# Kernel tuning notes

Hardware: AMD Instinct MI355X
Metric: run time of the kernel (lower is better)

The kernel has to match this reference:

```python
import jax, jax.numpy as jnp
import numpy as np

B, S, HID = 2, 2048, 2048
H, KVH, D = 16, 4, 128
GROUPS = H // KVH  # 4


def apply_rotary(x, cos, sin):
    # x: [B, h, S, D]; cos/sin: [S, D//2]
    xr = x[..., 0::2]
    xi = x[..., 1::2]
    c = cos[None, None, :, :]
    s = sin[None, None, :, :]
    orr = xr * c - xi * s
    oi = xr * s + xi * c
    return jnp.stack([orr, oi], axis=-1).reshape(x.shape)


def setup_inputs() -> dict:
    key = jax.random.key(0)
    k0, k1, k2, k3, k4 = jax.random.split(key, 5)
    x = jax.random.normal(k0, (B, S, HID), dtype=jnp.float32)
    # real RoPE frequencies (llama-style), stored as [S, D//2, 2] = (cos, sin)
    inv_freq = 1.0 / (10000.0 ** (np.arange(0, D, 2, dtype=np.float32) / D))
    t = np.arange(S, dtype=np.float32)
    ang = np.outer(t, inv_freq)  # [S, D//2]
    freqs_cis = jnp.asarray(np.stack([np.cos(ang), np.sin(ang)], axis=-1), dtype=jnp.float32)
    sc = 0.02
    wq = jax.random.normal(k1, (HID, H * D), dtype=jnp.float32) * sc
    wk = jax.random.normal(k2, (HID, KVH * D), dtype=jnp.float32) * sc
    wv = jax.random.normal(k3, (HID, KVH * D), dtype=jnp.float32) * sc
    wo = jax.random.normal(k4, (H * D, HID), dtype=jnp.float32) * sc
    return {"x": x, "freqs_cis": freqs_cis, "wq": wq, "wk": wk, "wv": wv, "wo": wo}


def reference(x, freqs_cis, wq, wk, wv, wo):
    b, s, _ = x.shape
    cos, sin = freqs_cis[..., 0], freqs_cis[..., 1]
    q = (x @ wq).reshape(b, s, H, D).transpose(0, 2, 1, 3)    # [B,H,S,D]
    k = (x @ wk).reshape(b, s, KVH, D).transpose(0, 2, 1, 3)  # [B,KVH,S,D]
    v = (x @ wv).reshape(b, s, KVH, D).transpose(0, 2, 1, 3)
    q = apply_rotary(q, cos, sin)
    k = apply_rotary(k, cos, sin)
    # GQA expand: repeat kv heads into query-head groups
    k = jnp.repeat(k, GROUPS, axis=1)  # [B,H,S,D]
    v = jnp.repeat(v, GROUPS, axis=1)
    scale = 1.0 / jnp.sqrt(jnp.asarray(D, dtype=x.dtype))
    scores = jnp.einsum("bhqd,bhkd->bhqk", q, k) * scale
    causal = jnp.tril(jnp.ones((s, s), dtype=bool))
    scores = jnp.where(causal[None, None], scores, jnp.asarray(-jnp.inf, dtype=scores.dtype))
    attn = jax.nn.softmax(scores, axis=-1)
    out = jnp.einsum("bhqk,bhkd->bhqd", attn, v)
    out = out.transpose(0, 2, 1, 3).reshape(b, s, H * D)
    return out @ wo
```

## Files before the change

### kernel.cpp

```cpp
#include <hip/hip_runtime.h>
#include <hip/hip_bf16.h>

#define B_   2
#define S_   2048
#define HID_ 2048
#define H_   16
#define KVH_ 4
#define D_   128
#define M_   4096
#define NQKV 3072

typedef __attribute__((ext_vector_type(8))) short bf16x8;
typedef __attribute__((ext_vector_type(4))) float f32x4;
typedef const __attribute__((address_space(1))) unsigned int* gas_p;
typedef __attribute__((address_space(3))) unsigned int* las_p;

__device__ __forceinline__ unsigned short f2b(float f) {
    __hip_bfloat16 h = __float2bfloat16(f);
    return *reinterpret_cast<unsigned short*>(&h);
}
__device__ __forceinline__ float b2f(unsigned short u) {
    __hip_bfloat16 h;
    *reinterpret_cast<unsigned short*>(&h) = u;
    return __bfloat162float(h);
}

__global__ __launch_bounds__(256)
void convert_all(const float* __restrict__ x,
                 const float* __restrict__ wq, const float* __restrict__ wk,
                 const float* __restrict__ wv, const float* __restrict__ wo,
                 unsigned short* __restrict__ xb,
                 unsigned short* __restrict__ wqkvT,
                 unsigned short* __restrict__ woT) {
    int z = blockIdx.z;
    if (z >= 4) {
        int lin = ((z - 4) * 64 + blockIdx.y) * 64 + blockIdx.x;
        int i = (lin * 256 + threadIdx.x) * 4;
        float4 v = *(const float4*)(x + i);
        ushort4 o;
        o.x = f2b(v.x); o.y = f2b(v.y); o.z = f2b(v.z); o.w = f2b(v.w);
        *(ushort4*)(xb + i) = o;
        return;
    }
    __shared__ float tile[32][33];
    const float* w; int N, nbase; unsigned short* dst;
    if (z == 0)      { w = wq; N = 2048; nbase = 0;    dst = wqkvT; }
    else if (z == 1) { w = wk; N = 512;  nbase = 2048; dst = wqkvT; }
    else if (z == 2) { w = wv; N = 512;  nbase = 2560; dst = wqkvT; }
    else             { w = wo; N = 2048; nbase = 0;    dst = woT; }
    int n0 = blockIdx.x * 32, k0 = blockIdx.y * 32;
    if (n0 >= N) return;
    int tx = threadIdx.x & 31, ty = threadIdx.x >> 5;
    #pragma unroll
    for (int j = 0; j < 4; j++)
        tile[ty + j*8][tx] = w[(size_t)(k0 + ty + j*8) * N + n0 + tx];
    __syncthreads();
    #pragma unroll
    for (int j = 0; j < 4; j++)
        dst[(size_t)(nbase + n0 + ty + j*8) * 2048 + k0 + tx] = f2b(tile[tx][ty + j*8]);
}

#define BAR    asm volatile("s_barrier" ::: "memory")
#define LG0    do { asm volatile("s_waitcnt lgkmcnt(0)" ::: "memory"); \
                    __builtin_amdgcn_sched_barrier(0); } while (0)
#define GATE0  asm volatile("s_waitcnt vmcnt(0)" ::: "memory")
#define GATE6  asm volatile("s_waitcnt vmcnt(6)" ::: "memory")
#define GATE7  asm volatile("s_waitcnt vmcnt(7)" ::: "memory")
#define PHI    __builtin_amdgcn_s_setprio(1)
#define PLO    __builtin_amdgcn_s_setprio(0)

#define STG(srcrow, ldsbase, half, tile) do {                                   \
    _Pragma("unroll")                                                           \
    for (int it_ = 0; it_ < 2; ++it_) {                                         \
      int p_ = w * 128 + it_ * 64 + lane;                                       \
      int r_ = (half) * 128 + (p_ >> 3);                                        \
      int q8_ = ((p_ & 7) ^ ((p_ >> 3) & 7)) * 8;                               \
      __builtin_amdgcn_global_load_lds(                                         \
          (gas_p)((srcrow) + (size_t)r_ * 2048 + (tile) * 64 + q8_),            \
          (las_p)((char*)(ldsbase) + ((half) * 1024 + w * 128 + it_ * 64) * 16),\
          16, 0, 0);                                                            \
    } } while (0)

#define STGB(srcrow, ldsbase, unit, tile) do {                                  \
      int p_ = w * 64 + lane;                                                   \
      int r_ = (unit) * 64 + (p_ >> 3);                                         \
      int q8_ = ((p_ & 7) ^ ((p_ >> 3) & 7)) * 8;                               \
      __builtin_amdgcn_global_load_lds(                                         \
          (gas_p)((srcrow) + (size_t)r_ * 2048 + (tile) * 64 + q8_),            \
          (las_p)((char*)(ldsbase) + ((unit) * 512 + p_) * 16),                 \
          16, 0, 0);                                                            \
    } while (0)

#define RDAq(dst, bufi) do {                                                    \
    const unsigned short* Ab_ = &As[bufi][0] + wr*4096 + l15*64;                \
    _Pragma("unroll")                                                           \
    for (int f_ = 0; f_ < 4; ++f_) {                                            \
      dst[f_][0] = *(const bf16x8*)(Ab_ + f_*1024 + slot0);                     \
      dst[f_][1] = *(const bf16x8*)(Ab_ + f_*1024 + slot1);                     \
    } } while (0)

#define RDBq(dst, bufi, nh) do {                                                \
    const unsigned short* Bb_ = &Bs[bufi][0] + wc*6144 + (nh)*3072 + l15*64;    \
    _Pragma("unroll")                                                           \
    for (int g_ = 0; g_ < 3; ++g_) {                                            \
      dst[g_][0] = *(const bf16x8*)(Bb_ + g_*1024 + slot0);                     \
      dst[g_][1] = *(const bf16x8*)(Bb_ + g_*1024 + slot1);                     \
    } } while (0)

#define MMq(mh, rb, nh) do {                                                    \
    _Pragma("unroll")                                                           \
    for (int f_ = 2*(mh); f_ < 2*(mh)+2; ++f_)                                  \
      _Pragma("unroll")                                                         \
      for (int g_ = 0; g_ < 3; ++g_) {                                          \
        acc[f_][(nh)*3+g_] = __builtin_amdgcn_mfma_f32_16x16x32_bf16(           \
            ra[f_][0], rb[g_][0], acc[f_][(nh)*3+g_], 0, 0, 0);                 \
        acc[f_][(nh)*3+g_] = __builtin_amdgcn_mfma_f32_16x16x32_bf16(           \
            ra[f_][1], rb[g_][1], acc[f_][(nh)*3+g_], 0, 0, 0);                 \
      } } while (0)

__global__ __launch_bounds__(512)
void gemm8(const unsigned short* __restrict__ A,
           const unsigned short* __restrict__ BT,
           unsigned short* __restrict__ qkvb,
           unsigned short* __restrict__ vTb,
           const float* __restrict__ freqs) {
    __shared__ unsigned short As[2][16384];
    __shared__ unsigned short Bs[2][12288];

    int tid  = threadIdx.x;
    int lane = tid & 63, w = tid >> 6;
    int l15  = lane & 15, quad = lane >> 4;
    int wr = w >> 1, wc = w & 1;
    int bid = blockIdx.y * 16 + blockIdx.x;
    int s_  = (bid & 7) * 32 + (bid >> 3);
    int by  = s_ >> 4, bx = s_ & 15;
    int row0 = by * 256, col0 = bx * 192;
    int slot0 = (quad ^ (lane & 7)) * 8;
    int slot1 = slot0 ^ 32;

    const unsigned short* Arow = A  + (size_t)row0 * 2048;
    const unsigned short* Brow = BT + (size_t)col0 * 2048;

    f32x4 acc[4][6];
    #pragma unroll
    for (int i = 0; i < 4; ++i)
        #pragma unroll
        for (int j = 0; j < 6; ++j) acc[i][j] = f32x4{0.f, 0.f, 0.f, 0.f};

    bf16x8 ra[4][2];
    bf16x8 rbl[3][2];
    bf16x8 rbh[3][2];

    STG (Arow, &As[0][0], 0, 0);
    STG (Arow, &As[0][0], 1, 0);
    STGB(Brow, &Bs[0][0], 0, 0);
    STGB(Brow, &Bs[0][0], 1, 0);
    STGB(Brow, &Bs[0][0], 2, 0);
    STG (Arow, &As[1][0], 0, 1);
    STG (Arow, &As[1][0], 1, 1);
    STGB(Brow, &Bs[1][0], 0, 1);
    STGB(Brow, &Bs[1][0], 1, 1);
    STGB(Brow, &Bs[1][0], 2, 1);
    GATE7;
    BAR;

    #pragma unroll 1
    for (int i = 0; i < 15; ++i) {
        int t = 2 * i;
        RDAq(ra, 0); RDBq(rbl, 0, 0);
        BAR; LG0; PHI; MMq(0, rbl, 0); PLO; BAR;
        RDBq(rbh, 0, 1); STG(Arow, &As[0][0], 0, t + 2);
        BAR; LG0; PHI; MMq(0, rbh, 1); PLO; BAR;
        STG(Arow, &As[0][0], 1, t + 2);
        BAR; LG0; PHI; MMq(1, rbl, 0); PLO; BAR;
        STGB(Brow, &Bs[0][0], 0, t + 2);
        STGB(Brow, &Bs[0][0], 1, t + 2);
        STGB(Brow, &Bs[0][0], 2, t + 2);
        BAR; LG0; PHI; MMq(1, rbh, 1); PLO; GATE7; BAR;
        RDAq(ra, 1); RDBq(rbl, 1, 0);
        BAR; LG0; PHI; MMq(0, rbl, 0); PLO; BAR;
        RDBq(rbh, 1, 1); STG(Arow, &As[1][0], 0, t + 3);
        BAR; LG0; PHI; MMq(0, rbh, 1); PLO; BAR;
        STG(Arow, &As[1][0], 1, t + 3);
        BAR; LG0; PHI; MMq(1, rbl, 0); PLO; BAR;
        STGB(Brow, &Bs[1][0], 0, t + 3);
        STGB(Brow, &Bs[1][0], 1, t + 3);
        STGB(Brow, &Bs[1][0], 2, t + 3);
        BAR; LG0; PHI; MMq(1, rbh, 1); PLO; GATE7; BAR;
    }
    RDAq(ra, 0); RDBq(rbl, 0, 0);
    BAR; LG0; PHI; MMq(0, rbl, 0); PLO; BAR;
    RDBq(rbh, 0, 1);
    BAR; LG0; PHI; MMq(0, rbh, 1); PLO; BAR;
    BAR; LG0; PHI; MMq(1, rbl, 0); PLO; BAR;
    BAR; LG0; PHI; MMq(1, rbh, 1); PLO; GATE0; BAR;
    RDAq(ra, 1); RDBq(rbl, 1, 0);
    BAR; LG0; PHI; MMq(0, rbl, 0); PLO; BAR;
    RDBq(rbh, 1, 1);
    BAR; LG0; PHI; MMq(0, rbh, 1); PLO; BAR;
    BAR; LG0; PHI; MMq(1, rbl, 0); PLO; BAR;
    LG0; PHI; MMq(1, rbh, 1); PLO;

    int q4 = quad * 4;
    const float qscale = 0.08838834764831845f;
    #pragma unroll
    for (int f = 0; f < 4; ++f) {
        int mb = row0 + wr*64 + f*16 + q4;
        #pragma unroll
        for (int g = 0; g < 6; ++g) {
            int colbase = col0 + wc*96 + g*16;
            int colb = colbase + l15;
            if (colbase < 2560) {
                int dd = (colb & 127) & ~1;
                bool odd = colb & 1;
                float sc = (colbase < 2048) ? qscale : 1.f;
                #pragma unroll
                for (int rr = 0; rr < 4; ++rr) {
                    int m = mb + rr;
                    int s = m & 2047;
                    float v  = acc[f][g][rr];
                    float pv = __shfl_xor(v, 1);
                    float cs = freqs[s*128 + dd];
                    float sn = freqs[s*128 + dd + 1];
                    float o  = odd ? (pv*sn + v*cs) : (v*cs - pv*sn);
                    qkvb[(size_t)m * NQKV + colb] = f2b(o * sc);
                }
            } else {
                int vrow = (row0 >> 11) * 512 + (colb - 2560);
                int s0 = mb & 2047;
                ushort4 ov;
                ov.x = f2b(acc[f][g][0]);
                ov.y = f2b(acc[f][g][1]);
                ov.z = f2b(acc[f][g][2]);
                ov.w = f2b(acc[f][g][3]);
                *(ushort4*)(vTb + (size_t)vrow * 2048 + s0) = ov;
            }
        }
    }
}

#define RDAo(bufi) do {                                                         \
    const unsigned short* Ab_ = &As[bufi][0] + wr * 4096 + l15 * 64;            \
    _Pragma("unroll")                                                           \
    for (int f_ = 0; f_ < 4; ++f_) {                                            \
      af[f_][0] = *(const bf16x8*)(Ab_ + f_ * 1024 + slot0);                    \
      af[f_][1] = *(const bf16x8*)(Ab_ + f_ * 1024 + slot1);                    \
    } } while (0)

#define RDBo(bufi, g) do {                                                      \
    const unsigned short* Bb_ = &Bs[bufi][0] + wc * 4096 + l15 * 64;            \
    bfr[g][0] = *(const bf16x8*)(Bb_ + (g) * 1024 + slot0);                     \
    bfr[g][1] = *(const bf16x8*)(Bb_ + (g) * 1024 + slot1);                     \
    } while (0)

#define MM8o(mi, ni) do {                                                       \
    _Pragma("unroll")                                                           \
    for (int f_ = 2*(mi); f_ < 2*(mi)+2; ++f_)                                  \
      _Pragma("unroll")                                                         \
      for (int g_ = 2*(ni); g_ < 2*(ni)+2; ++g_) {                              \
        acc[f_][g_] = __builtin_amdgcn_mfma_f32_16x16x32_bf16(                  \
            af[f_][0], bfr[g_][0], acc[f_][g_], 0, 0, 0);                       \
        acc[f_][g_] = __builtin_amdgcn_mfma_f32_16x16x32_bf16(                  \
            af[f_][1], bfr[g_][1], acc[f_][g_], 0, 0, 0);                       \
      } } while (0)

__global__ __launch_bounds__(512)
void gemm8o(const unsigned short* __restrict__ A,
            const unsigned short* __restrict__ BT,
            float* __restrict__ Cf) {
    __shared__ unsigned short As[2][16384];
    __shared__ unsigned short Bs[2][8192];

    int tid  = threadIdx.x;
    int lane = tid & 63, w = tid >> 6;
    int l15  = lane & 15, quad = lane >> 4;
    int wr = w >> 1, wc = w & 1;
    int bid = blockIdx.y * 16 + blockIdx.x;
    int s_  = (bid & 7) * 32 + (bid >> 3);
    int by  = s_ >> 4, bx = s_ & 15;
    int row0 = by * 256, col0 = bx * 128;
    int slot0 = (quad ^ (lane & 7)) * 8;
    int slot1 = slot0 ^ 32;

    const unsigned short* Arow = A  + (size_t)row0 * 2048;
    const unsigned short* Brow = BT + (size_t)col0 * 2048;

    f32x4 acc[4][4];
    #pragma unroll
    for (int i = 0; i < 4; ++i)
        #pragma unroll
        for (int j = 0; j < 4; ++j) acc[i][j] = f32x4{0.f, 0.f, 0.f, 0.f};

    bf16x8 af[4][2];
    bf16x8 bfr[4][2];

    STG(Arow, &As[0][0], 0, 0);
    STG(Arow, &As[0][0], 1, 0);
    STG(Brow, &Bs[0][0], 0, 0);
    STG(Arow, &As[1][0], 0, 1);
    STG(Arow, &As[1][0], 1, 1);
    STG(Brow, &Bs[1][0], 0, 1);
    GATE6;
    BAR;

    #pragma unroll 1
    for (int i = 0; i < 15; ++i) {
        int t = 2 * i;
        RDAo(0); RDBo(0, 0); RDBo(0, 1);
        BAR; LG0; PHI; MM8o(0, 0); PLO; BAR;
        RDBo(0, 2); RDBo(0, 3); STG(Arow, &As[0][0], 0, t + 2);
        BAR; LG0; PHI; MM8o(0, 1); PLO; BAR;
        STG(Arow, &As[0][0], 1, t + 2);
        BAR; LG0; PHI; MM8o(1, 0); PLO; BAR;
        STG(Brow, &Bs[0][0], 0, t + 2);
        BAR; LG0; PHI; MM8o(1, 1); PLO; GATE6; BAR;
        RDAo(1); RDBo(1, 0); RDBo(1, 1);
        BAR; LG0; PHI; MM8o(0, 0); PLO; BAR;
        RDBo(1, 2); RDBo(1, 3); STG(Arow, &As[1][0], 0, t + 3);
        BAR; LG0; PHI; MM8o(0, 1); PLO; BAR;
        STG(Arow, &As[1][0], 1, t + 3);
        BAR; LG0; PHI; MM8o(1, 0); PLO; BAR;
        STG(Brow, &Bs[1][0], 0, t + 3);
        BAR; LG0; PHI; MM8o(1, 1); PLO; GATE6; BAR;
    }
    RDAo(0); RDBo(0, 0); RDBo(0, 1);
    BAR; LG0; PHI; MM8o(0, 0); PLO; BAR;
    RDBo(0, 2); RDBo(0, 3);
    BAR; LG0; PHI; MM8o(0, 1); PLO; BAR;
    BAR; LG0; PHI; MM8o(1, 0); PLO; BAR;
    BAR; LG0; PHI; MM8o(1, 1); PLO; GATE0; BAR;
    RDAo(1); RDBo(1, 0); RDBo(1, 1);
    BAR; LG0; PHI; MM8o(0, 0); PLO; BAR;
    RDBo(1, 2); RDBo(1, 3);
    BAR; LG0; PHI; MM8o(0, 1); PLO; BAR;
    BAR; LG0; PHI; MM8o(1, 0); PLO; BAR;
    LG0; PHI; MM8o(1, 1); PLO;

    int q4 = quad * 4;
    #pragma unroll
    for (int f = 0; f < 4; ++f) {
        int mb = row0 + wr*64 + f*16 + q4;
        #pragma unroll
        for (int g = 0; g < 4; ++g) {
            int colb = col0 + wc*64 + g*16 + l15;
            #pragma unroll
            for (int rr = 0; rr < 4; ++rr)
                Cf[(size_t)(mb + rr) * 2048 + colb] = acc[f][g][rr];
        }
    }
}

__global__ __launch_bounds__(512)
void attn_mfma(const unsigned short* __restrict__ qkv,
               const unsigned short* __restrict__ vT,
               unsigned short* __restrict__ ao,
               unsigned short* __restrict__ wsP,
               float2* __restrict__ wsML) {
    __shared__ unsigned short Ks[64 * 128];
    __shared__ unsigned short Vt[128 * 64];

    int tid  = threadIdx.x;
    int lane = tid & 63, w = tid >> 6;
    int quad = lane >> 4, l15 = lane & 15;
    int hw = w >> 1, qhalf = w & 1;
    int bx = blockIdx.x, hk = blockIdx.y, b = blockIdx.z;
    int h = hk * 4 + hw;

    int qt, c;
    if (bx < 12)      { qt = 31 - bx / 3;        c = bx % 3; }
    else if (bx < 40) { qt = 27 - (bx - 12) / 2; c = (bx - 12) & 1; }
    else              { qt = 53 - bx;            c = 0; }
    int nt = qt + 1;
    int nch = (qt >= 28) ? 3 : (qt >= 14 ? 2 : 1);
    int kt_begin = c * 14;
    int kt_end = (nt < (c + 1) * 14) ? nt : (c + 1) * 14;
    bool lastc = (c == nch - 1);
    int q0 = qt * 64;

    bf16x8 aq[2][4];
    #pragma unroll
    for (int qf = 0; qf < 2; qf++) {
        const unsigned short* qrow =
            qkv + (size_t)(b*2048 + q0 + qhalf*32 + qf*16 + l15) * NQKV + h*128;
        #pragma unroll
        for (int k4 = 0; k4 < 4; k4++)
            aq[qf][k4] = *(const bf16x8*)(qrow + k4*32 + quad*8);
    }

    int koff[4][4];
    #pragma unroll
    for (int j = 0; j < 4; j++) {
        int row = ((j >> 1) * 32) + ((l15 >> 2) * 8) + ((j & 1) * 4) + (l15 & 3);
        #pragma unroll
        for (int k4 = 0; k4 < 4; k4++) {
            int slot = (k4 * 4 + quad) ^ (row & 15);
            koff[j][k4] = (row * 16 + slot) * 8;
        }
    }
    int vbase0 = (l15 * 8 + (quad ^ (l15 & 7))) * 8;
    int vbase1 = (l15 * 8 + ((4 + quad) ^ (l15 & 7))) * 8;

    const unsigned short* kb0 = qkv + (size_t)(b*2048) * NQKV + 2048 + hk*128;
    const unsigned short* vb0 = vT + (size_t)(b*512 + hk*128) * 2048;

    auto stage_k = [&](int kt) {
        #pragma unroll
        for (int it = 0; it < 2; it++) {
            int s = w * 128 + it * 64 + lane;
            int r = s >> 4, qp = s & 15;
            int q = qp ^ (r & 15);
            __builtin_amdgcn_global_load_lds(
                (gas_p)(kb0 + (size_t)(kt*64 + r) * NQKV + q * 8),
                (las_p)((char*)&Ks[0] + (w * 128 + it * 64) * 16),
                16, 0, 0);
        }
    };
    auto stage_v = [&](int kt) {
        #pragma unroll
        for (int it = 0; it < 2; it++) {
            int s = w * 128 + it * 64 + lane;
            int r = s >> 3, qp = s & 7;
            int q = qp ^ (r & 7);
            __builtin_amdgcn_global_load_lds(
                (gas_p)(vb0 + (size_t)r * 2048 + kt*64 + q * 8),
                (las_p)((char*)&Vt[0] + (w * 128 + it * 64) * 16),
                16, 0, 0);
        }
    };

    f32x4 o_acc[2][8];
    const f32x4 zf = {0.f, 0.f, 0.f, 0.f};
    #pragma unroll
    for (int qf = 0; qf < 2; qf++)
        #pragma unroll
        for (int jn = 0; jn < 8; jn++) o_acc[qf][jn] = zf;
    float m_i[2] = {-1e30f, -1e30f}, l_i[2] = {0.f, 0.f};
    int qglob[2] = {q0 + qhalf*32 + l15, q0 + qhalf*32 + 16 + l15};

    stage_k(kt_begin);
    for (int kt = kt_begin; kt < kt_end; kt++) {
        __syncthreads();
        stage_v(kt);

        f32x4 s_acc[2][4];
        #pragma unroll
        for (int j = 0; j < 4; j++) {
            s_acc[0][j] = zf; s_acc[1][j] = zf;
            #pragma unroll
            for (int k4 = 0; k4 < 4; k4++) {
                bf16x8 ak = *(const bf16x8*)&Ks[koff[j][k4]];
                s_acc[0][j] = __builtin_amdgcn_mfma_f32_16x16x32_bf16(ak, aq[0][k4], s_acc[0][j], 0, 0, 0);
                s_acc[1][j] = __builtin_amdgcn_mfma_f32_16x16x32_bf16(ak, aq[1][k4], s_acc[1][j], 0, 0, 0);
            }
        }

        bf16x8 pp[2][2];
        #pragma unroll
        for (int qf = 0; qf < 2; qf++) {
            float sv[4][4];
            #pragma unroll
            for (int j = 0; j < 4; j++)
                #pragma unroll
                for (int r = 0; r < 4; r++)
                    sv[j][r] = s_acc[qf][j][r];
            if (kt == qt) {
                #pragma unroll
                for (int j = 0; j < 4; j++)
                    #pragma unroll
                    for (int r = 0; r < 4; r++) {
                        int sloc = ((j >> 1) * 32) + quad*8 + ((j & 1) * 4) + r;
                        if (kt*64 + sloc > qglob[qf]) sv[j][r] = -1e30f;
                    }
            }
            float mx = sv[0][0];
            #pragma unroll
            for (int j = 0; j < 4; j++)
                #pragma unroll
                for (int r = 0; r < 4; r++) mx = fmaxf(mx, sv[j][r]);
            mx = fmaxf(mx, __shfl_xor(mx, 16));
            mx = fmaxf(mx, __shfl_xor(mx, 32));
            int defer = __all(mx <= m_i[qf] + 8.f);
            float mnew = defer ? m_i[qf] : fmaxf(m_i[qf], mx);
            float rs = 0.f;
            float p[4][4];
            #pragma unroll
            for (int j = 0; j < 4; j++)
                #pragma unroll
                for (int r = 0; r < 4; r++) {
                    p[j][r] = __expf(sv[j][r] - mnew);
                    rs += p[j][r];
                }
            if (!defer) {
                float alpha = __expf(m_i[qf] - mnew);
                l_i[qf] *= alpha;
                #pragma unroll
                for (int jn = 0; jn < 8; jn++)
                    #pragma unroll
                    for (int r = 0; r < 4; r++) o_acc[qf][jn][r] *= alpha;
                m_i[qf] = mnew;
            }
            l_i[qf] += rs;
            #pragma unroll
            for (int r = 0; r < 4; r++) {
                pp[qf][0][r]     = (short)f2b(p[0][r]);
                pp[qf][0][r + 4] = (short)f2b(p[1][r]);
                pp[qf][1][r]     = (short)f2b(p[2][r]);
                pp[qf][1][r + 4] = (short)f2b(p[3][r]);
            }
        }

        __syncthreads();
        if (kt + 1 < kt_end) stage_k(kt + 1);

        #pragma unroll
        for (int jn = 0; jn < 8; jn++) {
            bf16x8 av0 = *(const bf16x8*)&Vt[jn*1024 + vbase0];
            bf16x8 av1 = *(const bf16x8*)&Vt[jn*1024 + vbase1];
            o_acc[0][jn] = __builtin_amdgcn_mfma_f32_16x16x32_bf16(av0, pp[0][0], o_acc[0][jn], 0, 0, 0);
            o_acc[0][jn] = __builtin_amdgcn_mfma_f32_16x16x32_bf16(av1, pp[0][1], o_acc[0][jn], 0, 0, 0);
            o_acc[1][jn] = __builtin_amdgcn_mfma_f32_16x16x32_bf16(av0, pp[1][0], o_acc[1][jn], 0, 0, 0);
            o_acc[1][jn] = __builtin_amdgcn_mfma_f32_16x16x32_bf16(av1, pp[1][1], o_acc[1][jn], 0, 0, 0);
        }
    }

    int pi = 0, mi = 0;
    if (qt >= 14) {
        if (qt < 28) { mi = (qt - 14) * 2 + c;       pi = qt - 14; }
        else         { mi = 28 + (qt - 28) * 3 + c;  pi = 14 + (qt - 28) * 2 + c; }
    }
    #pragma unroll
    for (int qf = 0; qf < 2; qf++) {
        float lt = l_i[qf];
        lt += __shfl_xor(lt, 16);
        lt += __shfl_xor(lt, 32);
        float inv = 1.f / lt;
        int q_local = qhalf * 32 + qf * 16 + l15;
        unsigned short* dst;
        if (lastc)
            dst = ao + (size_t)(b*2048 + q0 + q_local) * 2048 + h*128;
        else
            dst = wsP + (size_t)(((pi * 8 + hk * 2 + b) * 4 + hw) * 64 + q_local) * 128;
        #pragma unroll
        for (int jn = 0; jn < 8; jn++) {
            ushort4 ov;
            ov.x = f2b(o_acc[qf][jn][0] * inv);
            ov.y = f2b(o_acc[qf][jn][1] * inv);
            ov.z = f2b(o_acc[qf][jn][2] * inv);
            ov.w = f2b(o_acc[qf][jn][3] * inv);
            *(ushort4*)(dst + jn*16 + quad*4) = ov;
        }
        if (qt >= 14 && quad == 0)
            wsML[(mi * 8 + hk * 2 + b) * 256 + hw * 64 + q_local]
                = make_float2(m_i[qf], lt);
    }
}

__global__ __launch_bounds__(256)
void merge_kernel(unsigned short* __restrict__ ao,
                  const unsigned short* __restrict__ wsP,
                  const float2* __restrict__ wsML) {
    int t = blockIdx.x * 256 + threadIdx.x;
    int d = (t & 15) * 8;
    int h = (t >> 4) & 15;
    int rest = t >> 8;
    int q_off = rest % 1152;
    int b = rest / 1152;
    int q = 896 + q_off;
    int qt = q >> 6, q_local = q & 63;
    int hk = h >> 2, hw = h & 3;
    int nch = (qt >= 28) ? 3 : 2;

    float mv[3], lv[3];
    for (int cc = 0; cc < nch; cc++) {
        int mi = (qt < 28) ? (qt - 14) * 2 + cc : 28 + (qt - 28) * 3 + cc;
        float2 ml = wsML[(mi * 8 + hk * 2 + b) * 256 + hw * 64 + q_local];
        mv[cc] = ml.x; lv[cc] = ml.y;
    }
    float M = mv[0];
    for (int cc = 1; cc < nch; cc++) M = fmaxf(M, mv[cc]);
    float f[3], S = 0.f;
    for (int cc = 0; cc < nch; cc++) { f[cc] = __expf(mv[cc] - M) * lv[cc]; S += f[cc]; }
    float inv = 1.f / S;

    unsigned short* arow = ao + (size_t)(b*2048 + q) * 2048 + h*128 + d;
    float outv[8];
    {
        ushort4 a0 = *(ushort4*)arow, a1 = *(ushort4*)(arow + 4);
        float fl = f[nch-1];
        outv[0] = fl*b2f(a0.x); outv[1] = fl*b2f(a0.y);
        outv[2] = fl*b2f(a0.z); outv[3] = fl*b2f(a0.w);
        outv[4] = fl*b2f(a1.x); outv[5] = fl*b2f(a1.y);
        outv[6] = fl*b2f(a1.z); outv[7] = fl*b2f(a1.w);
    }
    for (int cc = 0; cc < nch - 1; cc++) {
        int pi = (qt < 28) ? (qt - 14) : 14 + (qt - 28) * 2 + cc;
        const unsigned short* prow =
            wsP + (size_t)(((pi * 8 + hk * 2 + b) * 4 + hw) * 64 + q_local) * 128 + d;
        ushort4 p0 = *(const ushort4*)prow, p1 = *(const ushort4*)(prow + 4);
        float fc = f[cc];
        outv[0] += fc*b2f(p0.x); outv[1] += fc*b2f(p0.y);
        outv[2] += fc*b2f(p0.z); outv[3] += fc*b2f(p0.w);
        outv[4] += fc*b2f(p1.x); outv[5] += fc*b2f(p1.y);
        outv[6] += fc*b2f(p1.z); outv[7] += fc*b2f(p1.w);
    }
    ushort4 o0, o1;
    o0.x = f2b(outv[0]*inv); o0.y = f2b(outv[1]*inv);
    o0.z = f2b(outv[2]*inv); o0.w = f2b(outv[3]*inv);
    o1.x = f2b(outv[4]*inv); o1.y = f2b(outv[5]*inv);
    o1.z = f2b(outv[6]*inv); o1.w = f2b(outv[7]*inv);
    *(ushort4*)arow = o0;
    *(ushort4*)(arow + 4) = o1;
}

extern "C" void kernel_launch(void* const* d_in, const int* in_sizes, int n_in,
                              void* d_out, int out_size, void* d_ws, size_t ws_size,
                              hipStream_t stream) {
    const float* x     = (const float*)d_in[0];
    const float* freqs = (const float*)d_in[1];
    const float* wq    = (const float*)d_in[2];
    const float* wk    = (const float*)d_in[3];
    const float* wv    = (const float*)d_in[4];
    const float* wo    = (const float*)d_in[5];
    float* out = (float*)d_out;

    char* ws = (char*)d_ws;
    unsigned short* xbf    = (unsigned short*)(ws);
    unsigned short* aobuf  = (unsigned short*)(ws);
    unsigned short* wqkvT  = (unsigned short*)(ws + (16u<<20));
    unsigned short* woT    = (unsigned short*)(ws + (28u<<20));
    unsigned short* qkvbuf = (unsigned short*)(ws + (36u<<20));
    unsigned short* vTbuf  = (unsigned short*)(ws + (60u<<20));
    unsigned short* wsP  = (unsigned short*)(ws + (16u<<20));
    float2*         wsML = (float2*)(ws + (16u<<20) + 176u*65536u);

    convert_all<<<dim3(64, 64, 6), dim3(256), 0, stream>>>(
        x, wq, wk, wv, wo, xbf, wqkvT, woT);
    gemm8<<<dim3(16, 16), dim3(512), 0, stream>>>(
        xbf, wqkvT, qkvbuf, vTbuf, freqs);
    attn_mfma<<<dim3(54, 4, 2), dim3(512), 0, stream>>>(qkvbuf, vTbuf, aobuf, wsP, wsML);
    merge_kernel<<<2304, dim3(256), 0, stream>>>(aobuf, wsP, wsML);
    gemm8o<<<dim3(2048/128, M_/256), dim3(512), 0, stream>>>(aobuf, woT, out);
}
```

Before: 293.4 us.

## Double-buffer K/V tiles in attention with two-ahead async prefetch

The attention kernel's shared K and V tiles become two-slot ping-pong buffers. Both tiles are prefetched two iterations ahead with async global-to-LDS loads, and a vmcnt(4) wait before the barrier guarantees only the next tile has landed. This replaces the old scheme, where V was loaded at the start of each iteration and K between the softmax and PV phases, each behind a __syncthreads. The aim is to hide global-load latency behind the MFMA work. The cost is double the LDS footprint, which may reduce occupancy, plus redundant clamped loads on the final iterations of each chunk.

```diff
diff --git a/kernel.cpp b/kernel.cpp
--- a/kernel.cpp
+++ b/kernel.cpp
@@ -64,6 +64,7 @@
 #define LG0    do { asm volatile("s_waitcnt lgkmcnt(0)" ::: "memory"); \
                     __builtin_amdgcn_sched_barrier(0); } while (0)
 #define GATE0  asm volatile("s_waitcnt vmcnt(0)" ::: "memory")
+#define GATE4  asm volatile("s_waitcnt vmcnt(4)" ::: "memory")
 #define GATE6  asm volatile("s_waitcnt vmcnt(6)" ::: "memory")
 #define GATE7  asm volatile("s_waitcnt vmcnt(7)" ::: "memory")
 #define PHI    __builtin_amdgcn_s_setprio(1)
@@ -356,8 +357,8 @@
                unsigned short* __restrict__ ao,
                unsigned short* __restrict__ wsP,
                float2* __restrict__ wsML) {
-    __shared__ unsigned short Ks[64 * 128];
-    __shared__ unsigned short Vt[128 * 64];
+    __shared__ unsigned short Ks[2][64 * 128];
+    __shared__ unsigned short Vt[2][128 * 64];
 
     int tid  = threadIdx.x;
     int lane = tid & 63, w = tid >> 6;
@@ -403,7 +404,7 @@
     const unsigned short* kb0 = qkv + (size_t)(b*2048) * NQKV + 2048 + hk*128;
     const unsigned short* vb0 = vT + (size_t)(b*512 + hk*128) * 2048;
 
-    auto stage_k = [&](int kt) {
+    auto stage_k = [&](int bf, int kt) {
         #pragma unroll
         for (int it = 0; it < 2; it++) {
             int s = w * 128 + it * 64 + lane;
@@ -411,11 +412,11 @@
             int q = qp ^ (r & 15);
             __builtin_amdgcn_global_load_lds(
                 (gas_p)(kb0 + (size_t)(kt*64 + r) * NQKV + q * 8),
-                (las_p)((char*)&Ks[0] + (w * 128 + it * 64) * 16),
+                (las_p)((char*)&Ks[bf][0] + (w * 128 + it * 64) * 16),
                 16, 0, 0);
         }
     };
-    auto stage_v = [&](int kt) {
+    auto stage_v = [&](int bf, int kt) {
         #pragma unroll
         for (int it = 0; it < 2; it++) {
             int s = w * 128 + it * 64 + lane;
@@ -423,7 +424,7 @@
             int q = qp ^ (r & 7);
             __builtin_amdgcn_global_load_lds(
                 (gas_p)(vb0 + (size_t)r * 2048 + kt*64 + q * 8),
-                (las_p)((char*)&Vt[0] + (w * 128 + it * 64) * 16),
+                (las_p)((char*)&Vt[bf][0] + (w * 128 + it * 64) * 16),
                 16, 0, 0);
         }
     };
@@ -437,18 +438,21 @@
     float m_i[2] = {-1e30f, -1e30f}, l_i[2] = {0.f, 0.f};
     int qglob[2] = {q0 + qhalf*32 + l15, q0 + qhalf*32 + 16 + l15};
 
-    stage_k(kt_begin);
+    int kt1 = (kt_begin + 1 < kt_end) ? kt_begin + 1 : kt_begin;
+    stage_k(0, kt_begin); stage_v(0, kt_begin);
+    stage_k(1, kt1);      stage_v(1, kt1);
+    GATE4;
+    BAR;
+
+    int p = 0;
     for (int kt = kt_begin; kt < kt_end; kt++) {
-        __syncthreads();
-        stage_v(kt);
-
         f32x4 s_acc[2][4];
         #pragma unroll
         for (int j = 0; j < 4; j++) {
             s_acc[0][j] = zf; s_acc[1][j] = zf;
             #pragma unroll
             for (int k4 = 0; k4 < 4; k4++) {
-                bf16x8 ak = *(const bf16x8*)&Ks[koff[j][k4]];
+                bf16x8 ak = *(const bf16x8*)&Ks[p][koff[j][k4]];
                 s_acc[0][j] = __builtin_amdgcn_mfma_f32_16x16x32_bf16(ak, aq[0][k4], s_acc[0][j], 0, 0, 0);
                 s_acc[1][j] = __builtin_amdgcn_mfma_f32_16x16x32_bf16(ak, aq[1][k4], s_acc[1][j], 0, 0, 0);
             }
@@ -482,13 +486,13 @@
             int defer = __all(mx <= m_i[qf] + 8.f);
             float mnew = defer ? m_i[qf] : fmaxf(m_i[qf], mx);
             float rs = 0.f;
-            float p[4][4];
+            float pexp[4][4];
             #pragma unroll
             for (int j = 0; j < 4; j++)
                 #pragma unroll
                 for (int r = 0; r < 4; r++) {
-                    p[j][r] = __expf(sv[j][r] - mnew);
-                    rs += p[j][r];
+                    pexp[j][r] = __expf(sv[j][r] - mnew);
+                    rs += pexp[j][r];
                 }
             if (!defer) {
                 float alpha = __expf(m_i[qf] - mnew);
@@ -502,25 +506,29 @@
             l_i[qf] += rs;
             #pragma unroll
             for (int r = 0; r < 4; r++) {
-                pp[qf][0][r]     = (short)f2b(p[0][r]);
-                pp[qf][0][r + 4] = (short)f2b(p[1][r]);
-                pp[qf][1][r]     = (short)f2b(p[2][r]);
-                pp[qf][1][r + 4] = (short)f2b(p[3][r]);
+                pp[qf][0][r]     = (short)f2b(pexp[0][r]);
+                pp[qf][0][r + 4] = (short)f2b(pexp[1][r]);
+                pp[qf][1][r]     = (short)f2b(pexp[2][r]);
+                pp[qf][1][r + 4] = (short)f2b(pexp[3][r]);
             }
         }
 
-        __syncthreads();
-        if (kt + 1 < kt_end) stage_k(kt + 1);
-
         #pragma unroll
         for (int jn = 0; jn < 8; jn++) {
-            bf16x8 av0 = *(const bf16x8*)&Vt[jn*1024 + vbase0];
-            bf16x8 av1 = *(const bf16x8*)&Vt[jn*1024 + vbase1];
+            bf16x8 av0 = *(const bf16x8*)&Vt[p][jn*1024 + vbase0];
+            bf16x8 av1 = *(const bf16x8*)&Vt[p][jn*1024 + vbase1];
             o_acc[0][jn] = __builtin_amdgcn_mfma_f32_16x16x32_bf16(av0, pp[0][0], o_acc[0][jn], 0, 0, 0);
             o_acc[0][jn] = __builtin_amdgcn_mfma_f32_16x16x32_bf16(av1, pp[0][1], o_acc[0][jn], 0, 0, 0);
             o_acc[1][jn] = __builtin_amdgcn_mfma_f32_16x16x32_bf16(av0, pp[1][0], o_acc[1][jn], 0, 0, 0);
             o_acc[1][jn] = __builtin_amdgcn_mfma_f32_16x16x32_bf16(av1, pp[1][1], o_acc[1][jn], 0, 0, 0);
         }
+
+        BAR;
+        int ktn = (kt + 2 < kt_end) ? kt + 2 : kt_end - 1;
+        stage_k(p, ktn); stage_v(p, ktn);
+        GATE4;
+        BAR;
+        p ^= 1;
     }
 
     int pi = 0, mi = 0;
```

Result: no change. 292.7 us (-0.2%).
